# Optimization experiments

Hardware: AMD Instinct MI355X
Metric: run time of the kernel (lower is better)

## Reference

```python
import jax, jax.numpy as jnp
import numpy as np

SCALE = 0.1
TEMP = 1.0
LN_EPS = 1e-6
NORM_EPS = 1e-12  # torch F.normalize eps

def setup_inputs() -> dict:
    key = jax.random.key(0)
    k1, = jax.random.split(key, 1)
    x = jax.random.normal(k1, (8192, 512), dtype=jnp.float32)
    gamma = jnp.ones((512,), dtype=jnp.float32)
    beta = jnp.zeros((512,), dtype=jnp.float32)
    return {"x": x, "gamma": gamma, "beta": beta}

def reference(x, gamma, beta):
    # L2-normalize rows (torch F.normalize semantics: x / max(||x||, eps))
    norm = jnp.maximum(jnp.linalg.norm(x, axis=1, keepdims=True), NORM_EPS)
    xn = x / norm                                   # [N, d]
    sim = (xn @ xn.T) / TEMP                        # [N, N]
    # dual_norm: row softmax + column softmax
    sim = jax.nn.softmax(sim, axis=1) + jax.nn.softmax(sim, axis=0)
    x_neg = sim @ x                                 # [N, d]
    y = x - SCALE * x_neg
    # LayerNorm over last dim, eps=1e-6
    mean = jnp.mean(y, axis=-1, keepdims=True)
    var = jnp.mean(jnp.square(y - mean), axis=-1, keepdims=True)
    out = (y - mean) * jax.lax.rsqrt(var + LN_EPS) * gamma + beta
    return out
```

## Files before the change

### kernel.cpp

```cpp
#include <hip/hip_runtime.h>
#include <math.h>

#define NN 8192
#define DD 512

constexpr float SCALE_C = 0.1f;
constexpr float LN_EPS_C = 1e-6f;
constexpr float NORM_EPS_C = 1e-12f;
constexpr float CBIG = 32768.0f;
constexpr float INV_CBIG = 1.0f / 32768.0f;

typedef __attribute__((ext_vector_type(8))) short bf16x8;
typedef __attribute__((ext_vector_type(4))) float f32x4;

#define MFMA16(a, b, c) __builtin_amdgcn_mfma_f32_16x16x32_bf16((a), (b), (c), 0, 0, 0)
#define MFMA8(a, b, c)                                                        \
  __builtin_amdgcn_mfma_f32_16x16x32_fp8_fp8((long)(a), (long)(b), (c), 0, 0, 0)

#define GLL16(g, l)                                                        \
  __builtin_amdgcn_global_load_lds(                                        \
      (const __attribute__((address_space(1))) unsigned int*)(g),          \
      (__attribute__((address_space(3))) unsigned int*)(l), 16, 0, 0)

#define WAITV6() asm volatile("s_waitcnt vmcnt(6)" ::: "memory")
#define WAITV4() asm volatile("s_waitcnt vmcnt(4)" ::: "memory")
#define WAITV0() asm volatile("s_waitcnt vmcnt(0)" ::: "memory")
#define WAITLGKM0() asm volatile("s_waitcnt lgkmcnt(0)" ::: "memory")
#define FENCE() asm volatile("" ::: "memory")
#define BAR() __builtin_amdgcn_s_barrier()

__device__ inline unsigned short f2bf(float f) {
  unsigned int u = __builtin_bit_cast(unsigned int, f);
  unsigned int r = (u + 0x7FFFu + ((u >> 16) & 1u)) >> 16;
  return (unsigned short)r;
}

__device__ inline unsigned int f2fp8n(float f) {
  unsigned int a = __builtin_bit_cast(unsigned int, f);
  unsigned int r = a + 0x7FFFFu + ((a >> 20) & 1u);
  return (r >> 20) - 960u;
}

__device__ inline unsigned int f2fp8(float f) {
  unsigned int u = __builtin_bit_cast(unsigned int, f);
  unsigned int s = (u >> 24) & 0x80u;
  unsigned int a = u & 0x7fffffffu;
  if (a >= 0x3C800000u) {
    unsigned int r = a + 0x7FFFFu + ((a >> 20) & 1u);
    return s | ((r >> 20) - 960u);
  }
  float af = __builtin_bit_cast(float, a);
  return s | (unsigned int)(int)rintf(af * 512.0f);
}

__device__ inline float fp82f(unsigned int b) {
  return __builtin_bit_cast(float, (b + 960u) << 20);
}

__global__ __launch_bounds__(128) void k_prep(const float* __restrict__ x,
                                              unsigned short* __restrict__ xnb) {
  const int row = blockIdx.x;
  const int t = threadIdx.x;
  float4 v = ((const float4*)(x + (size_t)row * DD))[t];
  float ss = v.x * v.x + v.y * v.y + v.z * v.z + v.w * v.w;
#pragma unroll
  for (int off = 32; off; off >>= 1) ss += __shfl_down(ss, off);
  __shared__ float red[2];
  if ((t & 63) == 0) red[t >> 6] = ss;
  __syncthreads();
  float rn = 1.0f / fmaxf(sqrtf(red[0] + red[1]), NORM_EPS_C);
  ushort4 o;
  o.x = f2bf(v.x * rn);
  o.y = f2bf(v.y * rn);
  o.z = f2bf(v.z * rn);
  o.w = f2bf(v.w * rn);
  ((ushort4*)(xnb + (size_t)row * DD))[t] = o;
}

__global__ __launch_bounds__(256) void k_tr(const float* __restrict__ x,
                                            unsigned char* __restrict__ xT8) {
  __shared__ unsigned char T8[64][68];
  const int j0 = blockIdx.x * 64;
  const int d0 = blockIdx.y * 64;
  const int t = threadIdx.x;
#pragma unroll
  for (int q = 0; q < 4; ++q) {
    int f = t + q * 256;
    int r = f >> 4, c4 = f & 15;
    float4 v = *(const float4*)&x[(size_t)(j0 + r) * DD + d0 + c4 * 4];
    unsigned int w = f2fp8(v.x) | (f2fp8(v.y) << 8) | (f2fp8(v.z) << 16) |
                     (f2fp8(v.w) << 24);
    *(unsigned int*)&T8[r][c4 * 4] = w;
  }
  __syncthreads();
  {
    const int d = t >> 2, j16 = t & 3;
    unsigned int w[4];
#pragma unroll
    for (int p = 0; p < 4; ++p) {
      w[p] = (unsigned int)T8[j16 * 16 + p * 4 + 0][d] |
             ((unsigned int)T8[j16 * 16 + p * 4 + 1][d] << 8) |
             ((unsigned int)T8[j16 * 16 + p * 4 + 2][d] << 16) |
             ((unsigned int)T8[j16 * 16 + p * 4 + 3][d] << 24);
    }
    uint4 o = make_uint4(w[0], w[1], w[2], w[3]);
    *(uint4*)&xT8[(size_t)(d0 + d) * NN + j0 + j16 * 16] = o;
  }
}

__global__ __launch_bounds__(256, 4) void k_rowsumE(const unsigned short* __restrict__ xnb,
                                                    float* __restrict__ lpart,
                                                    unsigned char* __restrict__ E8) {
  __shared__ __align__(16) unsigned char POOL[24576];
  __shared__ float red[4][64];
  __shared__ float red2[4][64];

  int b = (blockIdx.x & 7) * 260 + (blockIdx.x >> 3);
  int bi = 0;
  while (b >= 64 - bi) { b -= 64 - bi; ++bi; }
  const int bj = bi + b;
  const int i0 = bi * 128, j0 = bj * 128;
  const int diag = (bi == bj);

  const int t = threadIdx.x;
  const int w = t >> 6, l = t & 63;
  const int lr = l & 15, lg = l >> 4;
  const int wr = w >> 1, wc = w & 1;
  const int r0 = w * 16 + (l >> 2);
  const int clog = (l & 3) ^ ((r0 >> 1) & 3);
  const unsigned short* gA = xnb + (size_t)(i0 + r0) * DD + clog * 8;
  const unsigned short* gBr = xnb + (size_t)(j0 + wc * 64 + lr) * DD + lg * 8;

#define RS_STAGE(s, kt)                                                        \
  do {                                                                         \
    GLL16(gA + (kt) * 32, (unsigned short*)(POOL + (s) * 8192) + w * 512);     \
    GLL16(gA + (size_t)64 * DD + (kt) * 32,                                    \
          (unsigned short*)(POOL + (s) * 8192 + 4096) + w * 512);              \
  } while (0)

#define B_LOAD(dst, kt)                                                        \
  do {                                                                         \
    _Pragma("unroll") for (int fn = 0; fn < 4; ++fn)(dst)[fn] =                \
        *(const bf16x8*)(gBr + (size_t)fn * 16 * DD + (kt) * 32);              \
  } while (0)

  RS_STAGE(0, 0);
  bf16x8 bv[2][4];
  B_LOAD(bv[0], 0);
  RS_STAGE(1, 1);

  f32x4 acc[4][4] = {};
#pragma unroll
  for (int ks = 0; ks < 16; ++ks) {
    if (ks == 15) { WAITV4(); } else { WAITV6(); }
    BAR(); FENCE();
    if (ks + 1 < 16) B_LOAD(bv[(ks + 1) & 1], ks + 1);
    if (ks + 2 < 16) RS_STAGE((ks + 2) % 3, ks + 2);
    const char* AS = (const char*)(POOL + (ks % 3) * 8192);
    __builtin_amdgcn_s_setprio(1);
#pragma unroll
    for (int fm = 0; fm < 4; ++fm) {
      const int row = wr * 64 + fm * 16 + lr;
      bf16x8 af = *(const bf16x8*)(AS + row * 64 + ((lg ^ ((row >> 1) & 3)) << 4));
#pragma unroll
      for (int fn = 0; fn < 4; ++fn)
        acc[fm][fn] = MFMA16(af, bv[ks & 1][fn], acc[fm][fn]);
    }
    __builtin_amdgcn_s_setprio(0);
  }
  BAR(); FENCE();

  unsigned int ebw[4][4];
  float rsum[4][4] = {};
  float csum[4] = {};
#pragma unroll
  for (int fm = 0; fm < 4; ++fm)
#pragma unroll
    for (int fn = 0; fn < 4; ++fn) {
      unsigned int pw = 0;
#pragma unroll
      for (int rr = 0; rr < 4; ++rr) {
        float e = __expf(acc[fm][fn][rr]);
        rsum[fm][rr] += e;
        csum[fn] += e;
        pw |= f2fp8n(e) << (8 * rr);
      }
      ebw[fm][fn] = pw;
    }

#pragma unroll
  for (int fm = 0; fm < 4; ++fm)
#pragma unroll
    for (int rr = 0; rr < 4; ++rr) {
      float s = rsum[fm][rr];
#pragma unroll
      for (int off = 1; off < 16; off <<= 1) s += __shfl_xor(s, off);
      if (lr == 0) red[w][fm * 16 + lg * 4 + rr] = s;
    }
  if (!diag) {
#pragma unroll
    for (int fn = 0; fn < 4; ++fn) {
      float cs = csum[fn];
      cs += __shfl_xor(cs, 16);
      cs += __shfl_xor(cs, 32);
      if (lg == 0) red2[w][fn * 16 + lr] = cs;
    }
  }

  unsigned char(*Et)[144] = (unsigned char(*)[144])POOL;
#pragma unroll
  for (int fm = 0; fm < 4; ++fm)
#pragma unroll
    for (int fn = 0; fn < 4; ++fn) {
#pragma unroll
      for (int rr = 0; rr < 4; ++rr)
        Et[wr * 64 + fm * 16 + lg * 4 + rr][wc * 64 + fn * 16 + lr] =
            (unsigned char)((ebw[fm][fn] >> (8 * rr)) & 0xffu);
    }
  __syncthreads();
  {
    unsigned char* dst = E8 + ((size_t)(bi * 64 + bj) << 14);
#pragma unroll
    for (int q = 0; q < 4; ++q) {
      const int f = t + q * 256;
      *(uint4*)(dst + f * 16) = *(const uint4*)&Et[f >> 3][(f & 7) * 16];
    }
  }
  if (t < 128) {
    const int wrx = t >> 6, idx = t & 63;
    lpart[(size_t)bj * NN + i0 + t] = red[2 * wrx][idx] + red[2 * wrx + 1][idx];
  } else if (!diag) {
    const int c = t - 128;
    const int wcx = c >> 6, idx = c & 63;
    lpart[(size_t)bi * NN + j0 + c] = red2[wcx][idx] + red2[2 + wcx][idx];
  }
}

__global__ __launch_bounds__(256) void k_recip(const float* __restrict__ lpart,
                                               float* __restrict__ rl) {
  const int i = blockIdx.x * 256 + threadIdx.x;
  float s = 0.f;
  for (int c = 0; c < 64; ++c) s += lpart[(size_t)c * NN + i];
  rl[i] = CBIG / s;
}

__global__ __launch_bounds__(256) void k_scale2(unsigned char* __restrict__ P,
                                                const float* __restrict__ rl) {
  __shared__ unsigned int T32[128][35];
  int b = blockIdx.x, ti = 0;
  while (b >= 64 - ti) { b -= 64 - ti; ++ti; }
  const int tj = ti + b;
  const int i0 = ti * 128, j0 = tj * 128;
  const int t = threadIdx.x;
  unsigned char* tileC = P + ((size_t)(ti * 64 + tj) << 14);

#pragma unroll
  for (int q = 0; q < 4; ++q) {
    const int f = t + q * 256;
    const int r = f >> 3;
    const int c0 = (f & 7) * 16;
    uint4 v = *(const uint4*)(tileC + f * 16);
    const float rli = rl[i0 + r];
    float rlj[16];
#pragma unroll
    for (int p = 0; p < 4; ++p) {
      float4 r4 = *(const float4*)(rl + j0 + c0 + p * 4);
      rlj[p * 4 + 0] = r4.x; rlj[p * 4 + 1] = r4.y;
      rlj[p * 4 + 2] = r4.z; rlj[p * 4 + 3] = r4.w;
    }
    unsigned int wsrc[4] = {v.x, v.y, v.z, v.w};
    unsigned int wdst[4];
#pragma unroll
    for (int p = 0; p < 4; ++p) {
      unsigned int in = wsrc[p], out = 0;
#pragma unroll
      for (int k = 0; k < 4; ++k) {
        float e = fp82f((in >> (8 * k)) & 0xffu);
        out |= f2fp8n(e * (rli + rlj[p * 4 + k])) << (8 * k);
      }
      wdst[p] = out;
      T32[r][(c0 >> 2) + p] = out;
    }
    *(uint4*)(tileC + f * 16) = make_uint4(wdst[0], wdst[1], wdst[2], wdst[3]);
  }
  if (ti == tj) return;
  __syncthreads();

  unsigned char* tileT = P + ((size_t)(tj * 64 + ti) << 14);
  {
    const int rg = t >> 3;
    const int cc = t & 7;
    const int c2 = cc * 16;
    unsigned int o[4][4];
#pragma unroll
    for (int k4 = 0; k4 < 4; ++k4) {
      unsigned int a0 = T32[c2 + k4 * 4 + 0][rg];
      unsigned int a1 = T32[c2 + k4 * 4 + 1][rg];
      unsigned int a2 = T32[c2 + k4 * 4 + 2][rg];
      unsigned int a3 = T32[c2 + k4 * 4 + 3][rg];
      unsigned int b0 = (a0 & 0x00FF00FFu) | ((a1 << 8) & 0xFF00FF00u);
      unsigned int b1 = ((a0 >> 8) & 0x00FF00FFu) | (a1 & 0xFF00FF00u);
      unsigned int b2 = (a2 & 0x00FF00FFu) | ((a3 << 8) & 0xFF00FF00u);
      unsigned int b3 = ((a2 >> 8) & 0x00FF00FFu) | (a3 & 0xFF00FF00u);
      o[0][k4] = (b0 & 0x0000FFFFu) | (b2 << 16);
      o[1][k4] = (b1 & 0x0000FFFFu) | (b3 << 16);
      o[2][k4] = (b0 >> 16) | (b2 & 0xFFFF0000u);
      o[3][k4] = (b1 >> 16) | (b3 & 0xFFFF0000u);
    }
#pragma unroll
    for (int i = 0; i < 4; ++i)
      *(uint4*)(tileT + (size_t)(rg * 4 + i) * 128 + c2) =
          make_uint4(o[i][0], o[i][1], o[i][2], o[i][3]);
  }
}

__global__ __launch_bounds__(256, 4) void k_pv3(const unsigned char* __restrict__ P8,
                                                const unsigned char* __restrict__ xT8,
                                                unsigned short* __restrict__ parts) {
  __shared__ __align__(16) unsigned char As[2][8192];
  __shared__ __align__(16) unsigned char Bs[2][8192];
  const int i0 = blockIdx.x * 128;
  const int n0 = blockIdx.y * 128;
  const int z = blockIdx.z;
  const int t = threadIdx.x;
  const int w = t >> 6, l = t & 63;
  const int lr = l & 15, lg = l >> 4;
  const int wr = w >> 1, wc = w & 1;
  const int r0 = w * 16 + (l >> 2);
  const int clog = (l & 3) ^ ((r0 >> 1) & 3);
  const unsigned char* Abase = P8 + ((size_t)((i0 >> 7) * 64 + z * 16) << 14) +
                               r0 * 128 + clog * 16;
  const unsigned char* gB = xT8 + (size_t)(n0 + r0) * NN + z * 2048 + clog * 16;

#define PV_STAGE(s, koff)                                                      \
  do {                                                                         \
    const unsigned char* a_ = Abase + (((koff) >> 7) << 14) + ((koff) & 127);  \
    GLL16(a_, &As[s][w * 1024]);                                               \
    GLL16(a_ + 8192, &As[s][4096 + w * 1024]);                                 \
    GLL16(gB + (koff), &Bs[s][w * 1024]);                                      \
    GLL16(gB + (size_t)64 * NN + (koff), &Bs[s][4096 + w * 1024]);             \
  } while (0)

  PV_STAGE(0, 0);
  PV_STAGE(1, 64);

  f32x4 acc[4][4] = {};
  for (int ks = 0; ks < 32; ++ks) {
    if (ks + 1 < 32) { WAITV4(); } else { WAITV0(); }
    BAR(); FENCE();
    const char* AS = (const char*)&As[ks & 1][0];
    const char* BS = (const char*)&Bs[ks & 1][0];
    unsigned long long af[4][2], bv[4][2];
#pragma unroll
    for (int fm = 0; fm < 4; ++fm) {
      const int row = wr * 64 + fm * 16 + lr;
      const int swz = (row >> 1) & 3;
#pragma unroll
      for (int kk = 0; kk < 2; ++kk) {
        int off = row * 64 + (((kk * 2 + (lg >> 1)) ^ swz) << 4) + ((lg & 1) << 3);
        af[fm][kk] = *(const unsigned long long*)(AS + off);
      }
    }
#pragma unroll
    for (int fn = 0; fn < 4; ++fn) {
      const int row = wc * 64 + fn * 16 + lr;
      const int swz = (row >> 1) & 3;
#pragma unroll
      for (int kk = 0; kk < 2; ++kk) {
        int off = row * 64 + (((kk * 2 + (lg >> 1)) ^ swz) << 4) + ((lg & 1) << 3);
        bv[fn][kk] = *(const unsigned long long*)(BS + off);
      }
    }
    WAITLGKM0();
    BAR(); FENCE();
    if (ks + 2 < 32) PV_STAGE(ks & 1, (ks + 2) * 64);
#pragma unroll
    for (int kk = 0; kk < 2; ++kk)
#pragma unroll
      for (int fm = 0; fm < 4; ++fm)
#pragma unroll
        for (int fn = 0; fn < 4; ++fn)
          acc[fm][fn] = MFMA8(af[fm][kk], bv[fn][kk], acc[fm][fn]);
  }
  unsigned short* dst = parts + (size_t)z * NN * DD;
#pragma unroll
  for (int fm = 0; fm < 4; ++fm)
#pragma unroll
    for (int fn = 0; fn < 4; ++fn)
#pragma unroll
      for (int rr = 0; rr < 4; ++rr)
        dst[(size_t)(i0 + wr * 64 + fm * 16 + lg * 4 + rr) * DD + n0 + wc * 64 +
            fn * 16 + lr] = f2bf(acc[fm][fn][rr] * INV_CBIG);
}

__global__ __launch_bounds__(128) void k_ln(const float* __restrict__ x,
                                            float* __restrict__ out,
                                            const unsigned short* __restrict__ parts,
                                            const float* __restrict__ gamma,
                                            const float* __restrict__ beta) {
  const int row = blockIdx.x;
  const int t = threadIdx.x;
  float4 p = make_float4(0.f, 0.f, 0.f, 0.f);
#pragma unroll
  for (int s = 0; s < 4; ++s) {
    ushort4 q = ((const ushort4*)(parts + (size_t)s * NN * DD + (size_t)row * DD))[t];
    p.x += __builtin_bit_cast(float, (unsigned int)q.x << 16);
    p.y += __builtin_bit_cast(float, (unsigned int)q.y << 16);
    p.z += __builtin_bit_cast(float, (unsigned int)q.z << 16);
    p.w += __builtin_bit_cast(float, (unsigned int)q.w << 16);
  }
  float4 xv = ((const float4*)(x + (size_t)row * DD))[t];
  float4 y;
  y.x = xv.x - SCALE_C * p.x;
  y.y = xv.y - SCALE_C * p.y;
  y.z = xv.z - SCALE_C * p.z;
  y.w = xv.w - SCALE_C * p.w;
  float sum = y.x + y.y + y.z + y.w;
#pragma unroll
  for (int off = 32; off; off >>= 1) sum += __shfl_down(sum, off);
  __shared__ float ra[2], rb[2];
  if ((t & 63) == 0) ra[t >> 6] = sum;
  __syncthreads();
  float mean = (ra[0] + ra[1]) * (1.0f / DD);
  float d0 = y.x - mean, d1 = y.y - mean, d2 = y.z - mean, d3 = y.w - mean;
  float vs = d0 * d0 + d1 * d1 + d2 * d2 + d3 * d3;
#pragma unroll
  for (int off = 32; off; off >>= 1) vs += __shfl_down(vs, off);
  if ((t & 63) == 0) rb[t >> 6] = vs;
  __syncthreads();
  float rstd = rsqrtf((rb[0] + rb[1]) * (1.0f / DD) + LN_EPS_C);
  float4 g4 = ((const float4*)gamma)[t];
  float4 b4 = ((const float4*)beta)[t];
  float4 o;
  o.x = d0 * rstd * g4.x + b4.x;
  o.y = d1 * rstd * g4.y + b4.y;
  o.z = d2 * rstd * g4.z + b4.z;
  o.w = d3 * rstd * g4.w + b4.w;
  ((float4*)(out + (size_t)row * DD))[t] = o;
}

extern "C" void kernel_launch(void* const* d_in, const int* in_sizes, int n_in,
                              void* d_out, int out_size, void* d_ws, size_t ws_size,
                              hipStream_t stream) {
  const float* x = (const float*)d_in[0];
  const float* gamma = (const float*)d_in[1];
  const float* beta = (const float*)d_in[2];
  float* out = (float*)d_out;

  unsigned short* xnb = (unsigned short*)d_ws;
  unsigned char* xT8 = (unsigned char*)(xnb + (size_t)NN * DD);
  float* lpart = (float*)(xT8 + (size_t)NN * DD);
  float* rl = lpart + (size_t)64 * NN;
  unsigned short* parts = (unsigned short*)(rl + NN);
  unsigned char* E8 = (unsigned char*)(parts + (size_t)4 * NN * DD);

  k_prep<<<NN, 128, 0, stream>>>(x, xnb);
  k_tr<<<dim3(NN / 64, DD / 64), 256, 0, stream>>>(x, xT8);
  k_rowsumE<<<2080, 256, 0, stream>>>(xnb, lpart, E8);
  k_recip<<<NN / 256, 256, 0, stream>>>(lpart, rl);
  k_scale2<<<2080, 256, 0, stream>>>(E8, rl);
  k_pv3<<<dim3(64, 4, 4), 256, 0, stream>>>(E8, xT8, parts);
  k_ln<<<NN, 128, 0, stream>>>(x, out, parts, gamma, beta);
}
```

Baseline: 181.6 us.

## Enlarge rowsumE tiles to 256x256 with 512 threads and LDS double buffering

The exp/row-sum kernel now computes 256x256 similarity tiles with 512 threads, up from 128x128 with 256 threads. Both A and B operands are staged into a 128KB XOR-swizzled LDS buffer through global_load_lds, double-buffered across k-steps, and the next stage's loads are interleaved with four MFMA phases. The aim is more operand reuse per byte loaded and fewer blocks and per-block overheads. The cost is low occupancy (the LDS footprint likely allows one block per CU), many more barriers, and redundant work on the lower-triangle quarter of diagonal tiles.

```diff
diff --git a/kernel.cpp b/kernel.cpp
--- a/kernel.cpp
+++ b/kernel.cpp
@@ -22,8 +22,8 @@
       (const __attribute__((address_space(1))) unsigned int*)(g),          \
       (__attribute__((address_space(3))) unsigned int*)(l), 16, 0, 0)
 
-#define WAITV6() asm volatile("s_waitcnt vmcnt(6)" ::: "memory")
 #define WAITV4() asm volatile("s_waitcnt vmcnt(4)" ::: "memory")
+#define WAITV2() asm volatile("s_waitcnt vmcnt(2)" ::: "memory")
 #define WAITV0() asm volatile("s_waitcnt vmcnt(0)" ::: "memory")
 #define WAITLGKM0() asm volatile("s_waitcnt lgkmcnt(0)" ::: "memory")
 #define FENCE() asm volatile("" ::: "memory")
@@ -108,73 +108,111 @@
   }
 }
 
-__global__ __launch_bounds__(256, 4) void k_rowsumE(const unsigned short* __restrict__ xnb,
+__global__ __launch_bounds__(512, 2) void k_rowsumE(const unsigned short* __restrict__ xnb,
                                                     float* __restrict__ lpart,
                                                     unsigned char* __restrict__ E8) {
-  __shared__ __align__(16) unsigned char POOL[24576];
-  __shared__ float red[4][64];
-  __shared__ float red2[4][64];
-
-  int b = (blockIdx.x & 7) * 260 + (blockIdx.x >> 3);
-  int bi = 0;
-  while (b >= 64 - bi) { b -= 64 - bi; ++bi; }
-  const int bj = bi + b;
-  const int i0 = bi * 128, j0 = bj * 128;
-  const int diag = (bi == bj);
+  __shared__ __align__(16) unsigned char POOL[131072];
+
+  int b = (blockIdx.x & 7) * 66 + (blockIdx.x >> 3);
+  int BI = 0;
+  while (b >= 32 - BI) { b -= 32 - BI; ++BI; }
+  const int BJ = BI + b;
+  const int i0 = BI * 256, j0 = BJ * 256;
+  const int diag = (BI == BJ);
 
   const int t = threadIdx.x;
   const int w = t >> 6, l = t & 63;
   const int lr = l & 15, lg = l >> 4;
-  const int wr = w >> 1, wc = w & 1;
-  const int r0 = w * 16 + (l >> 2);
-  const int clog = (l & 3) ^ ((r0 >> 1) & 3);
-  const unsigned short* gA = xnb + (size_t)(i0 + r0) * DD + clog * 8;
-  const unsigned short* gBr = xnb + (size_t)(j0 + wc * 64 + lr) * DD + lg * 8;
-
-#define RS_STAGE(s, kt)                                                        \
+  const int wr = w >> 2, wc = w & 3;
+
+#define ST_HALF(Rglob, LbOff, ktv)                                             \
   do {                                                                         \
-    GLL16(gA + (kt) * 32, (unsigned short*)(POOL + (s) * 8192) + w * 512);     \
-    GLL16(gA + (size_t)64 * DD + (kt) * 32,                                    \
-          (unsigned short*)(POOL + (s) * 8192 + 4096) + w * 512);              \
+    _Pragma("unroll") for (int q_ = 0; q_ < 2; ++q_) {                         \
+      const int f_ = q_ * 512 + t;                                             \
+      const int row_ = f_ >> 3, c_ = f_ & 7;                                   \
+      GLL16((const unsigned char*)xnb + (size_t)((Rglob) + row_) * 1024 +      \
+                (ktv) * 128 + ((c_ ^ (row_ & 7)) << 4),                        \
+            POOL + (LbOff) + q_ * 8192 + w * 1024);                            \
+    }                                                                          \
   } while (0)
 
-#define B_LOAD(dst, kt)                                                        \
-  do {                                                                         \
-    _Pragma("unroll") for (int fn = 0; fn < 4; ++fn)(dst)[fn] =                \
-        *(const bf16x8*)(gBr + (size_t)fn * 16 * DD + (kt) * 32);              \
-  } while (0)
-
-  RS_STAGE(0, 0);
-  bf16x8 bv[2][4];
-  B_LOAD(bv[0], 0);
-  RS_STAGE(1, 1);
-
-  f32x4 acc[4][4] = {};
-#pragma unroll
-  for (int ks = 0; ks < 16; ++ks) {
-    if (ks == 15) { WAITV4(); } else { WAITV6(); }
+  ST_HALF(i0, 0, 0);
+  ST_HALF(i0 + 128, 16384, 0);
+  ST_HALF(j0, 32768, 0);
+  ST_HALF(j0 + 128, 49152, 0);
+
+  f32x4 acc[8][4] = {};
+
+  for (int kt = 0; kt < 8; ++kt) {
+    const int buf = kt & 1;
+    const unsigned char* Ab = POOL + buf * 65536;
+    const unsigned char* Bb = Ab + 32768;
+    const int nx = (kt + 1 < 8);
+    const int nb = (buf ^ 1) * 65536;
+    bf16x8 bv[4][2];
+    bf16x8 af[2][2];
+
+    if (nx) ST_HALF(i0, nb + 0, kt + 1);
+    if (nx) { WAITV2(); } else { WAITV0(); }
     BAR(); FENCE();
-    if (ks + 1 < 16) B_LOAD(bv[(ks + 1) & 1], ks + 1);
-    if (ks + 2 < 16) RS_STAGE((ks + 2) % 3, ks + 2);
-    const char* AS = (const char*)(POOL + (ks % 3) * 8192);
+#pragma unroll
+    for (int fn = 0; fn < 4; ++fn) {
+      const int row = wc * 64 + fn * 16 + lr;
+#pragma unroll
+      for (int kk = 0; kk < 2; ++kk)
+        bv[fn][kk] = *(const bf16x8*)(Bb + row * 128 +
+                                      (((kk * 4 + lg) ^ (row & 7)) << 4));
+    }
+#pragma unroll
+    for (int fq = 0; fq < 2; ++fq) {
+      const int row = wr * 128 + fq * 16 + lr;
+#pragma unroll
+      for (int kk = 0; kk < 2; ++kk)
+        af[fq][kk] = *(const bf16x8*)(Ab + row * 128 +
+                                      (((kk * 4 + lg) ^ (row & 7)) << 4));
+    }
     __builtin_amdgcn_s_setprio(1);
 #pragma unroll
-    for (int fm = 0; fm < 4; ++fm) {
-      const int row = wr * 64 + fm * 16 + lr;
-      bf16x8 af = *(const bf16x8*)(AS + row * 64 + ((lg ^ ((row >> 1) & 3)) << 4));
-#pragma unroll
-      for (int fn = 0; fn < 4; ++fn)
-        acc[fm][fn] = MFMA16(af, bv[ks & 1][fn], acc[fm][fn]);
-    }
+    for (int kk = 0; kk < 2; ++kk)
+#pragma unroll
+      for (int fq = 0; fq < 2; ++fq)
+#pragma unroll
+        for (int fn = 0; fn < 4; ++fn)
+          acc[fq][fn] = MFMA16(af[fq][kk], bv[fn][kk], acc[fq][fn]);
     __builtin_amdgcn_s_setprio(0);
-  }
-  BAR(); FENCE();
-
-  unsigned int ebw[4][4];
-  float rsum[4][4] = {};
+    BAR(); FENCE();
+
+#define PHASE_P(p, stR, stL)                                                   \
+    do {                                                                       \
+      _Pragma("unroll") for (int fq = 0; fq < 2; ++fq) {                       \
+        const int row = wr * 128 + (2 * (p) + fq) * 16 + lr;                   \
+        _Pragma("unroll") for (int kk = 0; kk < 2; ++kk)                       \
+          af[fq][kk] = *(const bf16x8*)(Ab + row * 128 +                       \
+                                        (((kk * 4 + lg) ^ (row & 7)) << 4));   \
+      }                                                                        \
+      if (nx) ST_HALF(stR, nb + stL, kt + 1);                                  \
+      BAR(); FENCE();                                                          \
+      __builtin_amdgcn_s_setprio(1);                                           \
+      _Pragma("unroll") for (int kk = 0; kk < 2; ++kk)                         \
+        _Pragma("unroll") for (int fq = 0; fq < 2; ++fq)                       \
+          _Pragma("unroll") for (int fn = 0; fn < 4; ++fn)                     \
+            acc[2 * (p) + fq][fn] =                                            \
+                MFMA16(af[fq][kk], bv[fn][kk], acc[2 * (p) + fq][fn]);         \
+      __builtin_amdgcn_s_setprio(0);                                           \
+      BAR(); FENCE();                                                          \
+    } while (0)
+
+    PHASE_P(1, i0 + 128, 16384);
+    PHASE_P(2, j0, 32768);
+    PHASE_P(3, j0 + 128, 49152);
+#undef PHASE_P
+  }
+
+  unsigned int ebw[8][4];
+  float rsum[8][4] = {};
   float csum[4] = {};
 #pragma unroll
-  for (int fm = 0; fm < 4; ++fm)
+  for (int fm = 0; fm < 8; ++fm)
 #pragma unroll
     for (int fn = 0; fn < 4; ++fn) {
       unsigned int pw = 0;
@@ -188,14 +226,16 @@
       ebw[fm][fn] = pw;
     }
 
-#pragma unroll
-  for (int fm = 0; fm < 4; ++fm)
+  float* redrow = (float*)(POOL + 69632);
+  float* redcol = (float*)(POOL + 73728);
+#pragma unroll
+  for (int fm = 0; fm < 8; ++fm)
 #pragma unroll
     for (int rr = 0; rr < 4; ++rr) {
       float s = rsum[fm][rr];
 #pragma unroll
       for (int off = 1; off < 16; off <<= 1) s += __shfl_xor(s, off);
-      if (lr == 0) red[w][fm * 16 + lg * 4 + rr] = s;
+      if (lr == 0) redrow[(wr * 4 + wc) * 128 + fm * 16 + lg * 4 + rr] = s;
     }
   if (!diag) {
 #pragma unroll
@@ -203,36 +243,50 @@
       float cs = csum[fn];
       cs += __shfl_xor(cs, 16);
       cs += __shfl_xor(cs, 32);
-      if (lg == 0) red2[w][fn * 16 + lr] = cs;
-    }
-  }
-
-  unsigned char(*Et)[144] = (unsigned char(*)[144])POOL;
-#pragma unroll
-  for (int fm = 0; fm < 4; ++fm)
+      if (lg == 0) redcol[wr * 256 + wc * 64 + fn * 16 + lr] = cs;
+    }
+  }
+
+  unsigned char* Et = POOL;
+#pragma unroll
+  for (int fm = 0; fm < 8; ++fm)
 #pragma unroll
     for (int fn = 0; fn < 4; ++fn) {
+      const int col = wc * 64 + fn * 16 + lr;
+      const int rbase = wr * 128 + fm * 16 + lg * 4;
 #pragma unroll
       for (int rr = 0; rr < 4; ++rr)
-        Et[wr * 64 + fm * 16 + lg * 4 + rr][wc * 64 + fn * 16 + lr] =
+        Et[(rbase + rr) * 272 + col] =
             (unsigned char)((ebw[fm][fn] >> (8 * rr)) & 0xffu);
     }
   __syncthreads();
-  {
-    unsigned char* dst = E8 + ((size_t)(bi * 64 + bj) << 14);
-#pragma unroll
-    for (int q = 0; q < 4; ++q) {
-      const int f = t + q * 256;
-      *(uint4*)(dst + f * 16) = *(const uint4*)&Et[f >> 3][(f & 7) * 16];
-    }
-  }
-  if (t < 128) {
-    const int wrx = t >> 6, idx = t & 63;
-    lpart[(size_t)bj * NN + i0 + t] = red[2 * wrx][idx] + red[2 * wrx + 1][idx];
+
+#pragma unroll
+  for (int a = 0; a < 2; ++a)
+#pragma unroll
+    for (int bq = 0; bq < 2; ++bq) {
+      unsigned char* dst =
+          E8 + ((size_t)((2 * BI + a) * 64 + (2 * BJ + bq)) << 14);
+#pragma unroll
+      for (int q = 0; q < 2; ++q) {
+        const int f = q * 512 + t;
+        const int rr_ = f >> 3, cc_ = (f & 7) * 16;
+        *(uint4*)(dst + f * 16) =
+            *(const uint4*)&Et[(a * 128 + rr_) * 272 + bq * 128 + cc_];
+      }
+    }
+  if (t < 256) {
+    const int row = t & 127, wrx = t >> 7;
+    const float h0 = redrow[(wrx * 4 + 0) * 128 + row] +
+                     redrow[(wrx * 4 + 1) * 128 + row];
+    const float h1 = redrow[(wrx * 4 + 2) * 128 + row] +
+                     redrow[(wrx * 4 + 3) * 128 + row];
+    lpart[(size_t)(2 * BJ) * NN + i0 + wrx * 128 + row] = h0;
+    lpart[(size_t)(2 * BJ + 1) * NN + i0 + wrx * 128 + row] = h1;
   } else if (!diag) {
-    const int c = t - 128;
-    const int wcx = c >> 6, idx = c & 63;
-    lpart[(size_t)bi * NN + j0 + c] = red2[wcx][idx] + red2[2 + wcx][idx];
+    const int col = t - 256;
+    const float tot = redcol[col] + redcol[256 + col];
+    lpart[(size_t)(2 * BI + (col >> 7)) * NN + j0 + col] = tot;
   }
 }
 
@@ -456,7 +510,7 @@
 
   k_prep<<<NN, 128, 0, stream>>>(x, xnb);
   k_tr<<<dim3(NN / 64, DD / 64), 256, 0, stream>>>(x, xT8);
-  k_rowsumE<<<2080, 256, 0, stream>>>(xnb, lpart, E8);
+  k_rowsumE<<<528, 512, 0, stream>>>(xnb, lpart, E8);
   k_recip<<<NN / 256, 256, 0, stream>>>(lpart, rl);
   k_scale2<<<2080, 256, 0, stream>>>(E8, rl);
   k_pv3<<<dim3(64, 4, 4), 256, 0, stream>>>(E8, xT8, parts);
```

New measurement: 171.2 us. 1.06x faster.
